# Performance work log

Hardware: AMD Instinct MI355X
Metric: run time of the kernel (lower is better)

Reference implementation:

```python
import jax, jax.numpy as jnp
import numpy as np

N_NODES = 100000
N_EDGES = 1600000
FEAT = 512
CLS = 64
HID = 200  # each hop layer output width; 3 hops -> 600 concat


def spmm(row, col, vals, x):
    # out[r] = sum_{e: row[e]==r} vals[e] * x[col[e]]  -- sparse A @ x
    return jax.ops.segment_sum(x[col] * vals[:, None], row, num_segments=x.shape[0])


def setup_inputs() -> dict:
    key = jax.random.key(0)
    ks = jax.random.split(key, 12)
    adj_index = jax.random.randint(ks[0], (2, N_EDGES), 0, N_NODES, dtype=jnp.int64)
    # scale like a normalized adjacency (~1/avg_degree) to keep powers stable
    adj_values = jax.random.uniform(ks[1], (N_EDGES,), dtype=jnp.float32) * (1.0 / 16.0)
    features = jax.random.normal(ks[2], (N_NODES, FEAT), dtype=jnp.float32)
    s1 = (2.0 / (FEAT + HID)) ** 0.5
    s2 = (2.0 / (3 * HID + HID)) ** 0.5
    sf = (2.0 / (3 * HID + CLS)) ** 0.5
    W1 = jax.random.normal(ks[3], (3, FEAT, HID), dtype=jnp.float32) * s1
    b1 = jax.random.normal(ks[4], (3, HID), dtype=jnp.float32) * 0.01
    W2 = jax.random.normal(ks[5], (3, 3 * HID, HID), dtype=jnp.float32) * s2
    b2 = jax.random.normal(ks[6], (3, HID), dtype=jnp.float32) * 0.01
    Wfc = jax.random.normal(ks[7], (3 * HID, CLS), dtype=jnp.float32) * sf
    bfc = jax.random.normal(ks[8], (CLS,), dtype=jnp.float32) * 0.01
    return {"adj_index": adj_index, "adj_values": adj_values, "features": features,
            "W1": W1, "b1": b1, "W2": W2, "b2": b2, "Wfc": Wfc, "bfc": bfc}


def reference(adj_index, adj_values, features, W1, b1, W2, b2, Wfc, bfc):
    # Inference mode: dropout is identity.
    row, col = adj_index[0], adj_index[1]
    # upper (sparse) layers: linear + bias + relu, then (iterations-1) spmm hops
    outs1 = []
    for i in range(3):  # iterations = i + 1
        h = jax.nn.relu(features @ W1[i] + b1[i][None, :])
        for _ in range(i):
            h = spmm(row, col, adj_values, h)
        outs1.append(h)
    abstract1 = jnp.concatenate(outs1, axis=1)  # [N, 600]
    # bottom (dense) layers: linear, (iterations-1) spmm hops, then + bias
    outs2 = []
    for i in range(3):
        h = abstract1 @ W2[i]
        for _ in range(i):
            h = spmm(row, col, adj_values, h)
        h = h + b2[i][None, :]
        outs2.append(h)
    abstract2 = jnp.concatenate(outs2, axis=1)  # [N, 600]
    node_emb = abstract2 @ Wfc + bfc  # [N, CLS]
    predictions = jax.nn.log_softmax(node_emb, axis=1)
    return node_emb, predictions
```

## Files before the change

kernel.cpp:

```cpp
#include <hip/hip_runtime.h>

typedef unsigned short u16;
typedef unsigned int u32;
typedef __attribute__((ext_vector_type(8))) short short8;
typedef __attribute__((ext_vector_type(4))) float f32x4;
typedef __attribute__((ext_vector_type(4))) u32 u32x4;
typedef __attribute__((ext_vector_type(2))) u32 u32x2;

#define NN 100000
#define PAD 640

__device__ __forceinline__ float b2f(u16 u) {
    union { u32 i; float f; } v; v.i = ((u32)u) << 16; return v.f;
}
__device__ __forceinline__ u16 f2b(float f) {
    union { float f; u32 i; } v; v.f = f;
    u32 x = v.i;
    return (u16)((x + 0x7FFFu + ((x >> 16) & 1u)) >> 16);
}
__device__ __forceinline__ u32 pack2(float lo, float hi) {
    return (u32)f2b(lo) | ((u32)f2b(hi) << 16);
}
__device__ __forceinline__ float rdf(const void* p, size_t i, int f) {
    return f ? ((const float*)p)[i] : b2f(((const u16*)p)[i]);
}
__device__ __forceinline__ void gload16(const u16* g, u16* l) {
    __builtin_amdgcn_global_load_lds(
        (const __attribute__((address_space(1))) void*)g,
        (__attribute__((address_space(3))) void*)l, 16, 0, 0);
}

__global__ void probe_k(const int* __restrict__ idx,
                        const void* avals, const void* feats, const void* W1,
                        const void* b1, const void* W2, const void* b2,
                        const void* Wfc, const void* bfc,
                        int* __restrict__ flags) {
    if (blockIdx.x != 0 || threadIdx.x >= 64) return;
    int lane = threadIdx.x;
    int v0 = idx[2 * lane + 1];
    int v1 = idx[2 * (lane + 64) + 1];
    int ok = (v0 == 0 && v1 == 0);
    int allz = __all(ok);
    if (lane == 0) flags[0] = allz ? 1 : 0;
    const void* ts[8] = {avals, feats, W1, b1, W2, b2, Wfc, bfc};
    const int ns[8] = {256, 256, 256, 128, 256, 128, 256, 32};
    for (int t = 0; t < 8; ++t) {
        const u16* p = (const u16*)ts[t];
        int n = ns[t], bad = 0;
        for (int i = lane; i < n; i += 64) {
            int e = (p[2 * i] >> 7) & 0xFF;
            if (e >= 133) bad++;
        }
        for (int off = 32; off; off >>= 1) bad += __shfl_xor(bad, off, 64);
        if (lane == 0) flags[1 + t] = (bad * 8 >= n) ? 1 : 0;
    }
}

__device__ __forceinline__ int load_row(const int* idx, int E, int f, int e) {
    return f ? idx[2 * e] : idx[e];
}
__device__ __forceinline__ int load_col(const int* idx, int E, int f, int e) {
    return f ? idx[2 * E + 2 * e] : idx[E + e];
}

__global__ void prep_k(const void* __restrict__ W1, const void* __restrict__ W2,
                       const void* __restrict__ Wfc,
                       const void* __restrict__ b1, const void* __restrict__ b2,
                       const void* __restrict__ bfc,
                       u16* __restrict__ w1t, u16* __restrict__ w2t,
                       u16* __restrict__ wfct, float* __restrict__ biasf,
                       const int* __restrict__ flags) {
    int i = blockIdx.x * 256 + threadIdx.x;
    int job = blockIdx.y;
    if (job == 0) {
        if (i >= 640 * 512) return;
        int n = i >> 9, k = i & 511;
        float v = 0.f;
        if (n < 600) {
            int ib = n / 200, c = n % 200;
            v = rdf(W1, (size_t)ib * 102400 + (size_t)k * 200 + c, flags[3]);
        }
        w1t[i] = f2b(v);
    } else if (job == 1) {
        if (i >= 640 * 640) return;
        int n = i / 640, k = i % 640;
        float v = 0.f;
        if (n < 600 && k < 600) {
            int ib = n / 200, c = n % 200;
            v = rdf(W2, (size_t)ib * 120000 + (size_t)k * 200 + c, flags[5]);
        }
        w2t[i] = f2b(v);
    } else if (job == 2) {
        if (i >= 64 * 640) return;
        int n = i / 640, k = i % 640;
        float v = 0.f;
        if (k < 600) v = rdf(Wfc, (size_t)k * 64 + n, flags[7]);
        wfct[i] = f2b(v);
    } else if (job == 3) {
        if (i < 600) biasf[i] = rdf(b1, i, flags[4]);
        else if (i < 1200) biasf[i] = rdf(b2, i - 600, flags[6]);
        else if (i < 1264) biasf[i] = rdf(bfc, i - 1200, flags[8]);
    } else {
        if (i >= 64) return;
        int fb2 = flags[6], fwf = flags[7];
        float s = rdf(bfc, i, flags[8]);
        for (int k = 0; k < 200; ++k)
            s += rdf(b2, k, fb2) * rdf(Wfc, (size_t)k * 64 + i, fwf);
        biasf[1280 + i] = s;
    }
}

__device__ __forceinline__ int pad8(int c) { return (c + 7) & ~7; }

__global__ void count_k(const int* __restrict__ idx, int E, const int* __restrict__ flags,
                        int* __restrict__ counts) {
    int e = blockIdx.x * 256 + threadIdx.x;
    if (e >= E) return;
    int r = load_row(idx, E, flags[0], e);
    if ((u32)r >= NN) return;
    atomicAdd(&counts[r], 1);
}

__global__ void chunksum_k(const int* __restrict__ counts, int* __restrict__ chsum) {
    __shared__ int sm[256];
    int c = blockIdx.x, t = threadIdx.x;
    int base = c * 1024, s = 0;
    for (int i = t; i < 1024; i += 256) {
        int g = base + i;
        if (g < NN) s += pad8(counts[g]);
    }
    sm[t] = s; __syncthreads();
    for (int off = 128; off; off >>= 1) {
        if (t < off) sm[t] += sm[t + off];
        __syncthreads();
    }
    if (t == 0) chsum[c] = sm[0];
}

__global__ void chscan_k(const int* __restrict__ chsum, int nch, int* __restrict__ choff,
                         int* __restrict__ row_ptr, int E) {
    if (threadIdx.x == 0 && blockIdx.x == 0) {
        int run = 0;
        for (int c = 0; c < nch; ++c) { choff[c] = run; run += chsum[c]; }
        row_ptr[NN] = run;
    }
}

__global__ __launch_bounds__(1024) void scan_k(const int* __restrict__ counts,
                                               const int* __restrict__ choff,
                                               int* __restrict__ row_ptr,
                                               int* __restrict__ cursor) {
    __shared__ int sm[1024];
    int c = blockIdx.x, t = threadIdx.x;
    int g = c * 1024 + t;
    int v = (g < NN) ? pad8(counts[g]) : 0;
    sm[t] = v;
    __syncthreads();
    for (int off = 1; off < 1024; off <<= 1) {
        int add = (t >= off) ? sm[t - off] : 0;
        __syncthreads();
        sm[t] += add;
        __syncthreads();
    }
    if (g < NN) {
        int ex = choff[c] + sm[t] - v;
        row_ptr[g] = ex;
        cursor[g] = ex;
    }
}

__global__ void scatter_k(const int* __restrict__ idx, const void* __restrict__ avals, int E,
                          const int* __restrict__ flags, int* __restrict__ cursor,
                          int* __restrict__ edges) {
    int e = blockIdx.x * 256 + threadIdx.x;
    if (e >= E) return;
    int f = flags[0];
    int r = load_row(idx, E, f, e);
    if ((u32)r >= NN) return;
    int c = load_col(idx, E, f, e);
    if ((u32)c >= NN) c = 0;
    int p = atomicAdd(&cursor[r], 1);
    edges[2 * p] = c;
    ((float*)edges)[2 * p + 1] = rdf(avals, e, flags[1]);
}

__global__ void padfill_k(const int* __restrict__ cursor, const int* __restrict__ row_ptr,
                          int* __restrict__ edges) {
    int r = blockIdx.x * 256 + threadIdx.x;
    if (r >= NN) return;
    int p = cursor[r], e = row_ptr[r + 1];
    for (; p < e; ++p) {
        edges[2 * p] = 0;
        ((float*)edges)[2 * p + 1] = 0.f;
    }
}

__global__ __launch_bounds__(512) void gemm1_k(
    const void* __restrict__ A, const u16* __restrict__ Bt,
    u16* __restrict__ C, u16* __restrict__ Cc,
    const float* __restrict__ bias, const int* __restrict__ flags,
    int M, int K, int lda, int ldc) {
    __shared__ u16 As[256 * 32];
    __shared__ u16 Bs[128 * 32];
    const int tid = threadIdx.x;
    const int wave = tid >> 6, lane = tid & 63;

    const int nwg = gridDim.x;
    const int q = nwg >> 3, r8 = nwg & 7;
    const int xcd = blockIdx.x & 7, lo = blockIdx.x >> 3;
    const int wg = (xcd < r8 ? xcd * (q + 1) : r8 * (q + 1) + (xcd - r8) * q) + lo;
    const int bmi = wg / 5, bni = wg - bmi * 5;
    const int bm = bmi * 256, bn = bni * 128;

    const int wrow = (wave >> 1) * 64, wcol = (wave & 1) * 64;
    const int l15 = lane & 15, l4 = lane >> 4;
    f32x4 acc[4][4] = {};

    const int ff = flags[2];
    const int rowA0 = wave * 32 + (lane >> 2);
    const int rowA1 = rowA0 + 16;
    const int colE = (lane & 3) * 8;
    int gr0 = bm + rowA0; if (gr0 >= M) gr0 = M - 1;
    int gr1 = bm + rowA1; if (gr1 >= M) gr1 = M - 1;
    const float* a0f = (const float*)A + (size_t)gr0 * lda + colE;
    const float* a1f = (const float*)A + (size_t)gr1 * lda + colE;
    const u16* a0h = (const u16*)A + (size_t)gr0 * lda + colE;
    const u16* a1h = (const u16*)A + (size_t)gr1 * lda + colE;
    const int aoff0 = rowA0 * 32 + colE;
    const int aoff1 = rowA1 * 32 + colE;
    const int rowB = wave * 16 + (lane >> 2);
    const u16* bp = Bt + (size_t)(bn + rowB) * K + colE;
    u16* lB = Bs + wave * 512;

    for (int k0 = 0; k0 < K; k0 += 32) {
        __syncthreads();
        gload16(bp + k0, lB);
        short8 w0, w1;
        if (ff) {
            f32x4 x0 = *(const f32x4*)(a0f + k0);
            f32x4 x1 = *(const f32x4*)(a0f + k0 + 4);
            f32x4 y0 = *(const f32x4*)(a1f + k0);
            f32x4 y1 = *(const f32x4*)(a1f + k0 + 4);
#pragma unroll
            for (int t = 0; t < 4; ++t) {
                w0[t] = (short)f2b(x0[t]); w0[t + 4] = (short)f2b(x1[t]);
                w1[t] = (short)f2b(y0[t]); w1[t + 4] = (short)f2b(y1[t]);
            }
        } else {
            w0 = *(const short8*)(a0h + k0);
            w1 = *(const short8*)(a1h + k0);
        }
        *(short8*)&As[aoff0] = w0;
        *(short8*)&As[aoff1] = w1;
        __syncthreads();
        short8 af[4], bf[4];
#pragma unroll
        for (int t = 0; t < 4; ++t) {
            af[t] = *(const short8*)&As[(wrow + t * 16 + l15) * 32 + l4 * 8];
            bf[t] = *(const short8*)&Bs[(wcol + t * 16 + l15) * 32 + l4 * 8];
        }
#pragma unroll
        for (int mi = 0; mi < 4; ++mi)
#pragma unroll
            for (int ni = 0; ni < 4; ++ni)
                acc[mi][ni] = __builtin_amdgcn_mfma_f32_16x16x32_bf16(
                    af[mi], bf[ni], acc[mi][ni], 0, 0, 0);
    }

#pragma unroll
    for (int mi = 0; mi < 4; ++mi)
#pragma unroll
        for (int ni = 0; ni < 4; ++ni)
#pragma unroll
            for (int r4 = 0; r4 < 4; ++r4) {
                int row = bm + wrow + mi * 16 + l4 * 4 + r4;
                int col = bn + wcol + ni * 16 + l15;
                if (row < M) {
                    float v = acc[mi][ni][r4];
                    if (col < 600) v += bias[col];
                    v = fmaxf(v, 0.0f);
                    u16 b = f2b(v);
                    C[(size_t)row * ldc + col] = b;
                    if (col < 200 || col >= 600)
                        Cc[(size_t)row * ldc + col] = b;
                }
            }
}

__global__ __launch_bounds__(512) void gemm2_k(
    const u16* __restrict__ A, const u16* __restrict__ Bt,
    u16* __restrict__ C, int M, int K, int lda, int ldc) {
    __shared__ u16 As[256 * 32];
    __shared__ u16 Bs[128 * 32];
    const int tid = threadIdx.x;
    const int wave = tid >> 6, lane = tid & 63;

    const int nwg = gridDim.x;
    const int q = nwg >> 3, r8 = nwg & 7;
    const int xcd = blockIdx.x & 7, lo = blockIdx.x >> 3;
    const int wg = (xcd < r8 ? xcd * (q + 1) : r8 * (q + 1) + (xcd - r8) * q) + lo;
    const int bmi = wg / 5, bni = wg - bmi * 5;
    const int bm = bmi * 256, bn = bni * 128;

    const int wrow = (wave >> 1) * 64, wcol = (wave & 1) * 64;
    const int l15 = lane & 15, l4 = lane >> 4;
    f32x4 acc[4][4] = {};

    const int rowA0 = wave * 32 + (lane >> 2);
    const int rowA1 = rowA0 + 16;
    const int colE = (lane & 3) * 8;
    int gr0 = bm + rowA0; if (gr0 >= M) gr0 = M - 1;
    int gr1 = bm + rowA1; if (gr1 >= M) gr1 = M - 1;
    const u16* a0p = A + (size_t)gr0 * lda + colE;
    const u16* a1p = A + (size_t)gr1 * lda + colE;
    u16* lA0 = As + wave * 1024;
    u16* lA1 = As + wave * 1024 + 512;
    const int rowB = wave * 16 + (lane >> 2);
    const u16* bp = Bt + (size_t)(bn + rowB) * K + colE;
    u16* lB = Bs + wave * 512;

    for (int k0 = 0; k0 < K; k0 += 32) {
        __syncthreads();
        gload16(a0p + k0, lA0);
        gload16(a1p + k0, lA1);
        gload16(bp + k0, lB);
        __syncthreads();
        short8 af[4], bf[4];
#pragma unroll
        for (int t = 0; t < 4; ++t) {
            af[t] = *(const short8*)&As[(wrow + t * 16 + l15) * 32 + l4 * 8];
            bf[t] = *(const short8*)&Bs[(wcol + t * 16 + l15) * 32 + l4 * 8];
        }
#pragma unroll
        for (int mi = 0; mi < 4; ++mi)
#pragma unroll
            for (int ni = 0; ni < 4; ++ni)
                acc[mi][ni] = __builtin_amdgcn_mfma_f32_16x16x32_bf16(
                    af[mi], bf[ni], acc[mi][ni], 0, 0, 0);
    }

#pragma unroll
    for (int mi = 0; mi < 4; ++mi)
#pragma unroll
        for (int ni = 0; ni < 4; ++ni)
#pragma unroll
            for (int r4 = 0; r4 < 4; ++r4) {
                int row = bm + wrow + mi * 16 + l4 * 4 + r4;
                int col = bn + wcol + ni * 16 + l15;
                if (row < M)
                    C[(size_t)row * ldc + col] = f2b(acc[mi][ni][r4]);
            }
}

__global__ __launch_bounds__(256) void fc64_k(
    const u16* __restrict__ A0, const u16* __restrict__ A1,
    const u16* __restrict__ Bt,
    float* __restrict__ out_ne, float* __restrict__ out_pred,
    const float* __restrict__ bias, int M, int K, int lda) {
    __shared__ __align__(16) char ldsbuf[128 * 64 * 4];
    u16* As = (u16*)ldsbuf;
    u16* Bs = (u16*)(ldsbuf + 8192);
    float* smC = (float*)ldsbuf;

    const int tid = threadIdx.x;
    const int wave = tid >> 6, lane = tid & 63;
    const int bm = blockIdx.x * 128;
    const int wrow = (wave >> 1) * 64, wcol = (wave & 1) * 32;
    const int l15 = lane & 15, l4 = lane >> 4;
    f32x4 acc[4][2] = {};

    const int colE = (lane & 3) * 8;
    int gr0 = bm + wave * 32 + (lane >> 2); if (gr0 >= M) gr0 = M - 1;
    int gr1 = bm + wave * 32 + 16 + (lane >> 2); if (gr1 >= M) gr1 = M - 1;
    const u16* a0p0 = A0 + (size_t)gr0 * lda + colE;
    const u16* a0p1 = A1 + (size_t)gr0 * lda + colE;
    const u16* a1p0 = A0 + (size_t)gr1 * lda + colE;
    const u16* a1p1 = A1 + (size_t)gr1 * lda + colE;
    const u16* bp = Bt + (size_t)(wave * 16 + (lane >> 2)) * K + colE;
    u16* lA0 = As + wave * 1024;
    u16* lA1 = As + wave * 1024 + 512;
    u16* lB = Bs + wave * 512;

    for (int k0 = 0; k0 < K; k0 += 32) {
        const bool in0 = (k0 + colE) < 200;
        const u16* pa0 = in0 ? a0p0 : a0p1;
        const u16* pa1 = in0 ? a1p0 : a1p1;
        __syncthreads();
        gload16(pa0 + k0, lA0);
        gload16(pa1 + k0, lA1);
        gload16(bp + k0, lB);
        __syncthreads();
        short8 af[4], bf[2];
#pragma unroll
        for (int t = 0; t < 4; ++t)
            af[t] = *(const short8*)&As[(wrow + t * 16 + l15) * 32 + l4 * 8];
#pragma unroll
        for (int t = 0; t < 2; ++t)
            bf[t] = *(const short8*)&Bs[(wcol + t * 16 + l15) * 32 + l4 * 8];
#pragma unroll
        for (int mi = 0; mi < 4; ++mi)
#pragma unroll
            for (int ni = 0; ni < 2; ++ni)
                acc[mi][ni] = __builtin_amdgcn_mfma_f32_16x16x32_bf16(
                    af[mi], bf[ni], acc[mi][ni], 0, 0, 0);
    }

    __syncthreads();
#pragma unroll
    for (int mi = 0; mi < 4; ++mi)
#pragma unroll
        for (int ni = 0; ni < 2; ++ni)
#pragma unroll
            for (int r4 = 0; r4 < 4; ++r4) {
                int rl = wrow + mi * 16 + l4 * 4 + r4;
                int col = wcol + ni * 16 + l15;
                int row = bm + rl;
                float v = acc[mi][ni][r4] + bias[col];
                smC[rl * 64 + col] = v;
                if (row < M) out_ne[(size_t)row * 64 + col] = v;
            }
    __syncthreads();

    const int rl = tid >> 1, half = tid & 1;
    const int row = bm + rl;
    float vv[32];
#pragma unroll
    for (int k = 0; k < 32; ++k) {
        int c = half * 32 + ((k + rl) & 31);
        vv[k] = smC[rl * 64 + c];
    }
    float m = vv[0];
#pragma unroll
    for (int k = 1; k < 32; ++k) m = fmaxf(m, vv[k]);
    m = fmaxf(m, __shfl_xor(m, 1, 64));
    float s = 0.f;
#pragma unroll
    for (int k = 0; k < 32; ++k) s += expf(vv[k] - m);
    s += __shfl_xor(s, 1, 64);
    float lg = m + logf(s);
    if (row < M) {
#pragma unroll
        for (int k = 0; k < 32; ++k) {
            int c = half * 32 + ((k + rl) & 31);
            out_pred[(size_t)row * 64 + c] = vv[k] - lg;
        }
    }
}

__global__ __launch_bounds__(256) void spmm400_k(
    const int* __restrict__ row_ptr, const int* __restrict__ edges,
    const u16* __restrict__ X, u16* __restrict__ Y1, u16* __restrict__ Yt,
    const float* __restrict__ bias1) {
    int r = blockIdx.x * 4 + (threadIdx.x >> 6);
    if (r >= NN) return;
    int lane = threadIdx.x & 63;
    int s = row_ptr[r], e = row_ptr[r + 1];
    if (s < 0) s = 0;
    if (e < s) e = s;
    float a[8] = {0.f, 0.f, 0.f, 0.f, 0.f, 0.f, 0.f, 0.f};
    const bool act = lane < 50;
    const u32* xl = (const u32*)X + lane * 4;
    for (int i = s; i < e; i += 8) {
        int cc[8]; float vv[8];
#pragma unroll
        for (int j = 0; j < 4; ++j) {
            u32x4 p = *(const u32x4*)(edges + 2 * (size_t)(i + 2 * j));
            union { u32 u; float f; } w0, w1;
            cc[2 * j] = (int)p[0];     w0.u = p[1];
            cc[2 * j + 1] = (int)p[2]; w1.u = p[3];
            vv[2 * j] = w0.f; vv[2 * j + 1] = w1.f;
        }
        if (act) {
            u32x4 g[8];
#pragma unroll
            for (int j = 0; j < 8; ++j) {
                u32 c = (u32)cc[j]; if (c >= NN) c = 0;
                g[j] = *(const u32x4*)(xl + (size_t)c * 320);
            }
#pragma unroll
            for (int j = 0; j < 8; ++j) {
                float v = vv[j];
#pragma unroll
                for (int q = 0; q < 4; ++q) {
                    union { u32 i; float f; } lo, hi;
                    lo.i = g[j][q] << 16; hi.i = g[j][q] & 0xffff0000u;
                    a[2 * q] = fmaf(v, lo.f, a[2 * q]);
                    a[2 * q + 1] = fmaf(v, hi.f, a[2 * q + 1]);
                }
            }
        }
    }
    if (bias1 && lane < 25) {
#pragma unroll
        for (int q = 0; q < 8; ++q) a[q] += bias1[lane * 8 + q];
    }
    u32x4 o;
    o[0] = pack2(a[0], a[1]); o[1] = pack2(a[2], a[3]);
    o[2] = pack2(a[4], a[5]); o[3] = pack2(a[6], a[7]);
    if (lane < 25) {
        *(u32x4*)((u32*)Y1 + (size_t)r * 320 + lane * 4) = o;
    } else if (lane < 50) {
        *(u32x4*)((u32*)Yt + (size_t)r * 100 + (lane - 25) * 4) = o;
    }
}

__global__ __launch_bounds__(256) void spmm200_k(
    const int* __restrict__ row_ptr, const int* __restrict__ edges,
    const u16* __restrict__ X, int ldx,
    u16* __restrict__ Y, int ldy,
    const float* __restrict__ bias) {
    int r = blockIdx.x * 4 + (threadIdx.x >> 6);
    if (r >= NN) return;
    int lane = threadIdx.x & 63;
    int s = row_ptr[r], e = row_ptr[r + 1];
    if (s < 0) s = 0;
    if (e < s) e = s;
    float a[4] = {0.f, 0.f, 0.f, 0.f};
    const bool act = lane < 50;
    const int ldxw = ldx >> 1, ldyw = ldy >> 1;
    const u32* xl = (const u32*)X + lane * 2;
    for (int i = s; i < e; i += 8) {
        int cc[8]; float vv[8];
#pragma unroll
        for (int j = 0; j < 4; ++j) {
            u32x4 p = *(const u32x4*)(edges + 2 * (size_t)(i + 2 * j));
            union { u32 u; float f; } w0, w1;
            cc[2 * j] = (int)p[0];     w0.u = p[1];
            cc[2 * j + 1] = (int)p[2]; w1.u = p[3];
            vv[2 * j] = w0.f; vv[2 * j + 1] = w1.f;
        }
        if (act) {
            u32x2 g[8];
#pragma unroll
            for (int j = 0; j < 8; ++j) {
                u32 c = (u32)cc[j]; if (c >= NN) c = 0;
                g[j] = *(const u32x2*)(xl + (size_t)c * ldxw);
            }
#pragma unroll
            for (int j = 0; j < 8; ++j) {
                float v = vv[j];
#pragma unroll
                for (int q = 0; q < 2; ++q) {
                    union { u32 i; float f; } lo, hi;
                    lo.i = g[j][q] << 16; hi.i = g[j][q] & 0xffff0000u;
                    a[2 * q] = fmaf(v, lo.f, a[2 * q]);
                    a[2 * q + 1] = fmaf(v, hi.f, a[2 * q + 1]);
                }
            }
        }
    }
    if (bias && act) {
#pragma unroll
        for (int q = 0; q < 4; ++q) a[q] += bias[lane * 4 + q];
    }
    if (act) {
        u32x2 o;
        o[0] = pack2(a[0], a[1]); o[1] = pack2(a[2], a[3]);
        *(u32x2*)((u32*)Y + (size_t)r * ldyw + lane * 2) = o;
    }
}

extern "C" void kernel_launch(void* const* d_in, const int* in_sizes, int n_in,
                              void* d_out, int out_size, void* d_ws, size_t ws_size,
                              hipStream_t stream) {
    const int* adj_idx = (const int*)d_in[0];
    const void* adj_vals = d_in[1];
    const void* feats = d_in[2];
    const void* W1 = d_in[3];
    const void* b1 = d_in[4];
    const void* W2 = d_in[5];
    const void* b2 = d_in[6];
    const void* Wfc = d_in[7];
    const void* bfc = d_in[8];
    const int E = in_sizes[1];
    (void)n_in; (void)out_size; (void)ws_size;

    char* ws = (char*)d_ws;
    size_t off = 0;
    auto alloc = [&](size_t b) { size_t o = off; off += (b + 255) & ~(size_t)255; return o; };
    u16* buf0 = (u16*)(ws + alloc((size_t)NN * PAD * 2));
    u16* buf1 = (u16*)(ws + alloc((size_t)NN * PAD * 2));
    u16* hop = (u16*)(ws + alloc((size_t)NN * 200 * 2));
    u16* w1t = (u16*)(ws + alloc((size_t)640 * 512 * 2));
    u16* w2t = (u16*)(ws + alloc((size_t)640 * 640 * 2));
    u16* wfct = (u16*)(ws + alloc((size_t)64 * 640 * 2));
    float* biasf = (float*)(ws + alloc(1344 * 4));
    int* counts = (int*)(ws + alloc((size_t)NN * 4));
    int* cursor = (int*)(ws + alloc((size_t)NN * 4));
    int* row_ptr = (int*)(ws + alloc((size_t)(NN + 1) * 4));
    int* chsum = (int*)(ws + alloc(4096));
    int* choff = (int*)(ws + alloc(4096));
    int* flags = (int*)(ws + alloc(256));
    int* edgesS = (int*)(ws + alloc(((size_t)E + 8 * (size_t)NN) * 8));

    float* out_ne = (float*)d_out;
    float* out_pred = out_ne + (size_t)NN * 64;

    probe_k<<<1, 64, 0, stream>>>(adj_idx, adj_vals, feats, W1, b1, W2, b2, Wfc, bfc, flags);
    dim3 gp(1600, 5);
    prep_k<<<gp, 256, 0, stream>>>(W1, W2, Wfc, b1, b2, bfc, w1t, w2t, wfct, biasf, flags);

    hipMemsetAsync(counts, 0, NN * 4, stream);
    count_k<<<(E + 255) / 256, 256, 0, stream>>>(adj_idx, E, flags, counts);
    const int NCH = (NN + 1023) / 1024;
    chunksum_k<<<NCH, 256, 0, stream>>>(counts, chsum);
    chscan_k<<<1, 64, 0, stream>>>(chsum, NCH, choff, row_ptr, E);
    scan_k<<<NCH, 1024, 0, stream>>>(counts, choff, row_ptr, cursor);
    scatter_k<<<(E + 255) / 256, 256, 0, stream>>>(adj_idx, adj_vals, E, flags, cursor, edgesS);
    padfill_k<<<(NN + 255) / 256, 256, 0, stream>>>(cursor, row_ptr, edgesS);

    const int NWG = ((NN + 255) / 256) * 5;
    gemm1_k<<<NWG, 512, 0, stream>>>(feats, w1t, buf0, buf1, biasf, flags, NN, 512, 512, PAD);
    spmm400_k<<<(NN + 3) / 4, 256, 0, stream>>>(row_ptr, edgesS,
                                                buf0 + 200, buf1 + 200, hop, nullptr);
    spmm200_k<<<(NN + 3) / 4, 256, 0, stream>>>(row_ptr, edgesS,
                                                hop, 200, buf1 + 400, PAD, nullptr);
    gemm2_k<<<NWG, 512, 0, stream>>>(buf1, w2t, buf0, NN, PAD, PAD, PAD);
    spmm400_k<<<(NN + 3) / 4, 256, 0, stream>>>(row_ptr, edgesS,
                                                buf0 + 200, buf1 + 200, hop, biasf + 800);
    spmm200_k<<<(NN + 3) / 4, 256, 0, stream>>>(row_ptr, edgesS,
                                                hop, 200, buf1 + 400, PAD, biasf + 1000);
    fc64_k<<<(NN + 127) / 128, 256, 0, stream>>>(buf0, buf1, wfct, out_ne, out_pred,
                                                 biasf + 1280, NN, PAD, PAD);
}
```

Measured before the change: 1.481 ms.

## Double-buffer LDS tiles and swizzle layout in dense GEMM kernels

Both dense GEMM kernels now keep two LDS buffers, so the global loads for the next K tile are issued while MFMAs run on the current one. Explicit waitcnt and barrier instructions replace the two __syncthreads per iteration. The LDS tile layout is also changed to an XOR-swizzled, 16-row-group arrangement to cut bank conflicts on fragment reads. This doubles LDS use per block, which may lower occupancy, and relies on hand-written vmcnt counts being correct.

New measurement: 1.578 ms. 6.6% more time.

```diff
diff --git a/kernel.cpp b/kernel.cpp
--- a/kernel.cpp
+++ b/kernel.cpp
@@ -195,13 +195,14 @@
     }
 }
 
+
 __global__ __launch_bounds__(512) void gemm1_k(
     const void* __restrict__ A, const u16* __restrict__ Bt,
     u16* __restrict__ C, u16* __restrict__ Cc,
     const float* __restrict__ bias, const int* __restrict__ flags,
     int M, int K, int lda, int ldc) {
-    __shared__ u16 As[256 * 32];
-    __shared__ u16 Bs[128 * 32];
+    __shared__ u16 As[2][256 * 32];
+    __shared__ u16 Bs[2][128 * 32];
     const int tid = threadIdx.x;
     const int wave = tid >> 6, lane = tid & 63;
 
@@ -214,57 +215,111 @@
 
     const int wrow = (wave >> 1) * 64, wcol = (wave & 1) * 64;
     const int l15 = lane & 15, l4 = lane >> 4;
+    const int fidx = l4 * 128 + (l15 ^ l4) * 8;
+    const int ga = wrow >> 4, gb = wcol >> 4;
     f32x4 acc[4][4] = {};
 
     const int ff = flags[2];
-    const int rowA0 = wave * 32 + (lane >> 2);
-    const int rowA1 = rowA0 + 16;
-    const int colE = (lane & 3) * 8;
-    int gr0 = bm + rowA0; if (gr0 >= M) gr0 = M - 1;
-    int gr1 = bm + rowA1; if (gr1 >= M) gr1 = M - 1;
-    const float* a0f = (const float*)A + (size_t)gr0 * lda + colE;
-    const float* a1f = (const float*)A + (size_t)gr1 * lda + colE;
-    const u16* a0h = (const u16*)A + (size_t)gr0 * lda + colE;
-    const u16* a1h = (const u16*)A + (size_t)gr1 * lda + colE;
-    const int aoff0 = rowA0 * 32 + colE;
-    const int aoff1 = rowA1 * 32 + colE;
-    const int rowB = wave * 16 + (lane >> 2);
-    const u16* bp = Bt + (size_t)(bn + rowB) * K + colE;
-    u16* lB = Bs + wave * 512;
-
-    for (int k0 = 0; k0 < K; k0 += 32) {
-        __syncthreads();
-        gload16(bp + k0, lB);
-        short8 w0, w1;
-        if (ff) {
-            f32x4 x0 = *(const f32x4*)(a0f + k0);
-            f32x4 x1 = *(const f32x4*)(a0f + k0 + 4);
-            f32x4 y0 = *(const f32x4*)(a1f + k0);
-            f32x4 y1 = *(const f32x4*)(a1f + k0 + 4);
+    const int NT = K >> 5;
+    const int cb = lane >> 4;
+    const int r15b = (lane & 15) ^ cb;
+    const u16* bp = Bt + (size_t)(bn + wave * 16 + r15b) * K + cb * 8;
+    u16* lB0 = &Bs[0][wave * 512];
+    u16* lB1 = &Bs[1][wave * 512];
+
+    if (ff) {
+        const int r15a = lane & 15;
+        int gr0 = bm + wave * 32 + r15a; if (gr0 >= M) gr0 = M - 1;
+        int gr1 = bm + wave * 32 + 16 + r15a; if (gr1 >= M) gr1 = M - 1;
+        const float* a0f = (const float*)A + (size_t)gr0 * lda + cb * 8;
+        const float* a1f = (const float*)A + (size_t)gr1 * lda + cb * 8;
+        const int d0 = (wave * 2) * 512 + cb * 128 + (r15a ^ cb) * 8;
+        const int d1 = d0 + 512;
+        f32x4 xa0, xa1, xb0, xb1;
+        auto loadA = [&](int k0) {
+            xa0 = *(const f32x4*)(a0f + k0); xa1 = *(const f32x4*)(a0f + k0 + 4);
+            xb0 = *(const f32x4*)(a1f + k0); xb1 = *(const f32x4*)(a1f + k0 + 4);
+        };
+        auto writeA = [&](int p) {
+            short8 w0, w1;
 #pragma unroll
             for (int t = 0; t < 4; ++t) {
-                w0[t] = (short)f2b(x0[t]); w0[t + 4] = (short)f2b(x1[t]);
-                w1[t] = (short)f2b(y0[t]); w1[t + 4] = (short)f2b(y1[t]);
-            }
-        } else {
-            w0 = *(const short8*)(a0h + k0);
-            w1 = *(const short8*)(a1h + k0);
-        }
-        *(short8*)&As[aoff0] = w0;
-        *(short8*)&As[aoff1] = w1;
-        __syncthreads();
-        short8 af[4], bf[4];
-#pragma unroll
-        for (int t = 0; t < 4; ++t) {
-            af[t] = *(const short8*)&As[(wrow + t * 16 + l15) * 32 + l4 * 8];
-            bf[t] = *(const short8*)&Bs[(wcol + t * 16 + l15) * 32 + l4 * 8];
-        }
-#pragma unroll
-        for (int mi = 0; mi < 4; ++mi)
-#pragma unroll
-            for (int ni = 0; ni < 4; ++ni)
-                acc[mi][ni] = __builtin_amdgcn_mfma_f32_16x16x32_bf16(
-                    af[mi], bf[ni], acc[mi][ni], 0, 0, 0);
+                w0[t] = (short)f2b(xa0[t]); w0[t + 4] = (short)f2b(xa1[t]);
+                w1[t] = (short)f2b(xb0[t]); w1[t + 4] = (short)f2b(xb1[t]);
+            }
+            *(short8*)&As[p][d0] = w0;
+            *(short8*)&As[p][d1] = w1;
+        };
+        gload16(bp, lB0);
+        loadA(0);
+        asm volatile("s_waitcnt vmcnt(0)" ::: "memory");
+        writeA(0);
+        loadA(32);
+        asm volatile("s_waitcnt lgkmcnt(0)" ::: "memory");
+        __builtin_amdgcn_s_barrier();
+        for (int t = 0; t < NT; ++t) {
+            const int p = t & 1;
+            if (t + 1 < NT) {
+                gload16(bp + (t + 1) * 32, p ? lB0 : lB1);
+                asm volatile("s_waitcnt vmcnt(1)" ::: "memory");
+                writeA(p ^ 1);
+                if (t + 2 < NT) loadA((t + 2) * 32);
+            } else {
+                asm volatile("s_waitcnt vmcnt(0)" ::: "memory");
+            }
+            __builtin_amdgcn_s_barrier();
+            short8 af[4], bf[4];
+#pragma unroll
+            for (int tt = 0; tt < 4; ++tt) {
+                af[tt] = *(const short8*)&As[p][(ga + tt) * 512 + fidx];
+                bf[tt] = *(const short8*)&Bs[p][(gb + tt) * 512 + fidx];
+            }
+#pragma unroll
+            for (int mi = 0; mi < 4; ++mi)
+#pragma unroll
+                for (int ni = 0; ni < 4; ++ni)
+                    acc[mi][ni] = __builtin_amdgcn_mfma_f32_16x16x32_bf16(
+                        af[mi], bf[ni], acc[mi][ni], 0, 0, 0);
+            asm volatile("s_waitcnt lgkmcnt(0)" ::: "memory");
+            __builtin_amdgcn_s_barrier();
+        }
+    } else {
+        const int r15x = (lane & 15) ^ cb;
+        int ra0 = bm + wave * 32 + r15x; if (ra0 >= M) ra0 = M - 1;
+        int ra1 = bm + wave * 32 + 16 + r15x; if (ra1 >= M) ra1 = M - 1;
+        const u16* a0h = (const u16*)A + (size_t)ra0 * lda + cb * 8;
+        const u16* a1h = (const u16*)A + (size_t)ra1 * lda + cb * 8;
+        u16* lA[2] = { &As[0][wave * 1024], &As[1][wave * 1024] };
+        gload16(a0h, lA[0]);
+        gload16(a1h, lA[0] + 512);
+        gload16(bp, lB0);
+        for (int t = 0; t < NT; ++t) {
+            const int p = t & 1;
+            if (t + 1 < NT) {
+                const int k1 = (t + 1) * 32;
+                gload16(a0h + k1, lA[p ^ 1]);
+                gload16(a1h + k1, lA[p ^ 1] + 512);
+                gload16(bp + k1, p ? lB0 : lB1);
+                asm volatile("s_waitcnt vmcnt(3)" ::: "memory");
+            } else {
+                asm volatile("s_waitcnt vmcnt(0)" ::: "memory");
+            }
+            __builtin_amdgcn_s_barrier();
+            short8 af[4], bf[4];
+#pragma unroll
+            for (int tt = 0; tt < 4; ++tt) {
+                af[tt] = *(const short8*)&As[p][(ga + tt) * 512 + fidx];
+                bf[tt] = *(const short8*)&Bs[p][(gb + tt) * 512 + fidx];
+            }
+#pragma unroll
+            for (int mi = 0; mi < 4; ++mi)
+#pragma unroll
+                for (int ni = 0; ni < 4; ++ni)
+                    acc[mi][ni] = __builtin_amdgcn_mfma_f32_16x16x32_bf16(
+                        af[mi], bf[ni], acc[mi][ni], 0, 0, 0);
+            asm volatile("s_waitcnt lgkmcnt(0)" ::: "memory");
+            __builtin_amdgcn_s_barrier();
+        }
     }
 
 #pragma unroll
@@ -290,8 +345,8 @@
 __global__ __launch_bounds__(512) void gemm2_k(
     const u16* __restrict__ A, const u16* __restrict__ Bt,
     u16* __restrict__ C, int M, int K, int lda, int ldc) {
-    __shared__ u16 As[256 * 32];
-    __shared__ u16 Bs[128 * 32];
+    __shared__ u16 As[2][256 * 32];
+    __shared__ u16 Bs[2][128 * 32];
     const int tid = threadIdx.x;
     const int wave = tid >> 6, lane = tid & 63;
 
@@ -304,32 +359,41 @@
 
     const int wrow = (wave >> 1) * 64, wcol = (wave & 1) * 64;
     const int l15 = lane & 15, l4 = lane >> 4;
+    const int fidx = l4 * 128 + (l15 ^ l4) * 8;
+    const int ga = wrow >> 4, gb = wcol >> 4;
     f32x4 acc[4][4] = {};
 
-    const int rowA0 = wave * 32 + (lane >> 2);
-    const int rowA1 = rowA0 + 16;
-    const int colE = (lane & 3) * 8;
-    int gr0 = bm + rowA0; if (gr0 >= M) gr0 = M - 1;
-    int gr1 = bm + rowA1; if (gr1 >= M) gr1 = M - 1;
-    const u16* a0p = A + (size_t)gr0 * lda + colE;
-    const u16* a1p = A + (size_t)gr1 * lda + colE;
-    u16* lA0 = As + wave * 1024;
-    u16* lA1 = As + wave * 1024 + 512;
-    const int rowB = wave * 16 + (lane >> 2);
-    const u16* bp = Bt + (size_t)(bn + rowB) * K + colE;
-    u16* lB = Bs + wave * 512;
-
-    for (int k0 = 0; k0 < K; k0 += 32) {
-        __syncthreads();
-        gload16(a0p + k0, lA0);
-        gload16(a1p + k0, lA1);
-        gload16(bp + k0, lB);
-        __syncthreads();
+    const int NT = K >> 5;
+    const int cb = lane >> 4;
+    const int r15x = (lane & 15) ^ cb;
+    int ra0 = bm + wave * 32 + r15x; if (ra0 >= M) ra0 = M - 1;
+    int ra1 = bm + wave * 32 + 16 + r15x; if (ra1 >= M) ra1 = M - 1;
+    const u16* a0h = A + (size_t)ra0 * lda + cb * 8;
+    const u16* a1h = A + (size_t)ra1 * lda + cb * 8;
+    const u16* bp = Bt + (size_t)(bn + wave * 16 + r15x) * K + cb * 8;
+    u16* lA[2] = { &As[0][wave * 1024], &As[1][wave * 1024] };
+    u16* lB[2] = { &Bs[0][wave * 512], &Bs[1][wave * 512] };
+
+    gload16(a0h, lA[0]);
+    gload16(a1h, lA[0] + 512);
+    gload16(bp, lB[0]);
+    for (int t = 0; t < NT; ++t) {
+        const int p = t & 1;
+        if (t + 1 < NT) {
+            const int k1 = (t + 1) * 32;
+            gload16(a0h + k1, lA[p ^ 1]);
+            gload16(a1h + k1, lA[p ^ 1] + 512);
+            gload16(bp + k1, lB[p ^ 1]);
+            asm volatile("s_waitcnt vmcnt(3)" ::: "memory");
+        } else {
+            asm volatile("s_waitcnt vmcnt(0)" ::: "memory");
+        }
+        __builtin_amdgcn_s_barrier();
         short8 af[4], bf[4];
 #pragma unroll
-        for (int t = 0; t < 4; ++t) {
-            af[t] = *(const short8*)&As[(wrow + t * 16 + l15) * 32 + l4 * 8];
-            bf[t] = *(const short8*)&Bs[(wcol + t * 16 + l15) * 32 + l4 * 8];
+        for (int tt = 0; tt < 4; ++tt) {
+            af[tt] = *(const short8*)&As[p][(ga + tt) * 512 + fidx];
+            bf[tt] = *(const short8*)&Bs[p][(gb + tt) * 512 + fidx];
         }
 #pragma unroll
         for (int mi = 0; mi < 4; ++mi)
@@ -337,6 +401,8 @@
             for (int ni = 0; ni < 4; ++ni)
                 acc[mi][ni] = __builtin_amdgcn_mfma_f32_16x16x32_bf16(
                     af[mi], bf[ni], acc[mi][ni], 0, 0, 0);
+        asm volatile("s_waitcnt lgkmcnt(0)" ::: "memory");
+        __builtin_amdgcn_s_barrier();
     }
 
 #pragma unroll
```
